# Performance work log

Measured on AMD Instinct MI355X. Metric: run time of the kernel, lower is better.

The kernel has to match this reference:

```python
import jax, jax.numpy as jnp
import numpy as np

B, T, I, H, O = 512, 2048, 4, 100, 1


def setup_inputs() -> dict:
    key = jax.random.key(0)
    k1, k2, k3, k4 = jax.random.split(key, 4)
    s_ih = 1.0 / np.sqrt(H)
    return {
        "x": jax.random.normal(k1, (B, T, I), dtype=jnp.float32),
        "W_ih": jax.random.uniform(k2, (H, I), minval=-s_ih, maxval=s_ih, dtype=jnp.float32),
        "W_hh": jax.random.uniform(k3, (H, H), minval=-s_ih, maxval=s_ih, dtype=jnp.float32),
        "W_fc": jax.random.uniform(k4, (O, H), minval=-s_ih, maxval=s_ih, dtype=jnp.float32),
        "b_fc": jnp.zeros((O,), dtype=jnp.float32),
    }


def reference(x, W_ih, W_hh, W_fc, b_fc):
    # Precompute input projections for all timesteps: [T, B, H]
    xp = jnp.einsum("bti,hi->tbh", x, W_ih)
    h0 = jnp.zeros((x.shape[0], W_hh.shape[0]), dtype=x.dtype)

    def step(h, xp_t):
        h_new = jnp.tanh(xp_t + h @ W_hh.T)
        return h_new, h_new

    _, hs = jax.lax.scan(step, h0, xp)          # hs: [T, B, H]
    hs = jnp.swapaxes(hs, 0, 1)                 # [B, T, H]
    out = jnp.einsum("bth,oh->bto", hs, W_fc) + b_fc  # [B, T, O]
    return out
```

## Files before the change

### kernel.cpp

```cpp
#include <hip/hip_runtime.h>


#define BB 512
#define TT 2048
#define II 4
#define HH 100
#define HP 104
#define CHUNK 64
#define NCH (TT / CHUNK)

__global__ __launch_bounds__(128, 1) void crnn_kernel(
    const float* __restrict__ x,
    const float* __restrict__ W_ih,
    const float* __restrict__ W_hh,
    const float* __restrict__ W_fc,
    const float* __restrict__ b_fc,
    float* __restrict__ out)
{
    __shared__ float xs[TT * II];
    __shared__ float hh[(CHUNK + 1) * HP];
    __shared__ float wfcs[HP];
    __shared__ float pt[2][CHUNK];

    const int tid = threadIdx.x;
    const int b   = blockIdx.x;
    const int j   = tid;
    const int jj  = (j < HH) ? j : HH - 1;
    const bool active = (j < HH);

    const float4* xg = reinterpret_cast<const float4*>(x + (size_t)b * TT * II);
    float4* xl = reinterpret_cast<float4*>(xs);
#pragma unroll
    for (int it = 0; it < (TT * II / 4) / 128; ++it)
        xl[it * 128 + tid] = xg[it * 128 + tid];

    float4 wih = reinterpret_cast<const float4*>(W_ih)[jj];
    float wr[HH];
    const float4* wrow = reinterpret_cast<const float4*>(W_hh + jj * HH);
#pragma unroll
    for (int k4 = 0; k4 < HH / 4; ++k4) {
        float4 v = wrow[k4];
        wr[4 * k4 + 0] = v.x; wr[4 * k4 + 1] = v.y;
        wr[4 * k4 + 2] = v.z; wr[4 * k4 + 3] = v.w;
    }
    if (tid < HP) wfcs[tid] = (tid < HH) ? W_fc[tid] : 0.f;
    const float bias = b_fc[0];
    if (tid < HP) hh[tid] = 0.f;
    for (int i = tid; i < (CHUNK + 1) * 4; i += 128) {
        int r = i >> 2, p = i & 3;
        hh[r * HP + HH + p] = 0.f;
    }
    __syncthreads();

    float* outb = out + (size_t)b * TT;
    const float4* xs4 = reinterpret_cast<const float4*>(xs);

    for (int c = 0; c < NCH; ++c) {
        for (int t = 0; t < CHUNK; ++t) {
            const float4* hrow = reinterpret_cast<const float4*>(hh + t * HP);
            float4 hv[HH / 4];
#pragma unroll
            for (int k4 = 0; k4 < HH / 4; ++k4) hv[k4] = hrow[k4];
            float4 xv = xs4[c * CHUNK + t];

            float a0 = wih.x * xv.x;
            float a1 = wih.y * xv.y;
            float a2 = wih.z * xv.z;
            float a3 = wih.w * xv.w;
#pragma unroll
            for (int k4 = 0; k4 < HH / 4; ++k4) {
                a0 = fmaf(wr[4 * k4 + 0], hv[k4].x, a0);
                a1 = fmaf(wr[4 * k4 + 1], hv[k4].y, a1);
                a2 = fmaf(wr[4 * k4 + 2], hv[k4].z, a2);
                a3 = fmaf(wr[4 * k4 + 3], hv[k4].w, a3);
            }
            float acc = (a0 + a1) + (a2 + a3);
            float e  = __expf(2.f * acc);
            float hn = 1.f - 2.f * __builtin_amdgcn_rcpf(e + 1.f);
            if (active) hh[(t + 1) * HP + j] = hn;
            __syncthreads();
        }

        const int tl = tid & (CHUNK - 1);
        const int kh = tid >> 6;
        const int k0 = kh * 52;
        const float4* wf4 = reinterpret_cast<const float4*>(wfcs + k0);
        const float4* hr  = reinterpret_cast<const float4*>(hh + (tl + 1) * HP + k0);
        float csum = 0.f;
#pragma unroll
        for (int i = 0; i < 13; ++i) {
            float4 hvv = hr[i];
            float4 wv  = wf4[i];
            csum = fmaf(hvv.x, wv.x, csum);
            csum = fmaf(hvv.y, wv.y, csum);
            csum = fmaf(hvv.z, wv.z, csum);
            csum = fmaf(hvv.w, wv.w, csum);
        }
        pt[kh][tl] = csum;
        if (tid < HH) hh[tid] = hh[CHUNK * HP + tid];
        __syncthreads();
        if (tid < CHUNK) outb[c * CHUNK + tid] = (pt[0][tid] + pt[1][tid]) + bias;
        __syncthreads();
    }
}

extern "C" void kernel_launch(void* const* d_in, const int* in_sizes, int n_in,
                              void* d_out, int out_size, void* d_ws, size_t ws_size,
                              hipStream_t stream) {
    const float* x    = (const float*)d_in[0];
    const float* W_ih = (const float*)d_in[1];
    const float* W_hh = (const float*)d_in[2];
    const float* W_fc = (const float*)d_in[3];
    const float* b_fc = (const float*)d_in[4];
    float* out = (float*)d_out;
    crnn_kernel<<<BB, 128, 0, stream>>>(x, W_ih, W_hh, W_fc, b_fc, out);
}
```

Baseline: 1.104 ms.

## Broadcast hidden state via wave readlane instead of LDS row reads

Each thread keeps its own new hidden value in a register, and the other wave's values come from a single LDS load per step. Both are broadcast to all lanes with readlane, which replaces the 25 float4 LDS reads of the whole hidden row per timestep. The hh buffer drops its extra carry row, and the copy of the last row plus one barrier per chunk are removed. The cost is about 100 scalar readlane operations on the serial dependency chain, and the padding is widened to 116.

```diff
diff --git a/kernel.cpp b/kernel.cpp
--- a/kernel.cpp
+++ b/kernel.cpp
@@ -5,9 +5,13 @@
 #define TT 2048
 #define II 4
 #define HH 100
-#define HP 104
+#define HP 116
 #define CHUNK 64
 #define NCH (TT / CHUNK)
+
+__device__ __forceinline__ float rlf(float v, int l) {
+    return __int_as_float(__builtin_amdgcn_readlane(__float_as_int(v), l));
+}
 
 __global__ __launch_bounds__(128, 1) void crnn_kernel(
     const float* __restrict__ x,
@@ -18,15 +22,17 @@
     float* __restrict__ out)
 {
     __shared__ float xs[TT * II];
-    __shared__ float hh[(CHUNK + 1) * HP];
+    __shared__ float hh[CHUNK * HP];
     __shared__ float wfcs[HP];
     __shared__ float pt[2][CHUNK];
 
-    const int tid = threadIdx.x;
-    const int b   = blockIdx.x;
-    const int j   = tid;
-    const int jj  = (j < HH) ? j : HH - 1;
-    const bool active = (j < HH);
+    const int tid  = threadIdx.x;
+    const int b    = blockIdx.x;
+    const int lane = tid & 63;
+    const int w    = tid >> 6;
+    const int j    = tid;
+    const int jj   = (j < HH) ? j : HH - 1;
+    const bool act = (j < HH);
 
     const float4* xg = reinterpret_cast<const float4*>(x + (size_t)b * TT * II);
     float4* xl = reinterpret_cast<float4*>(xs);
@@ -45,47 +51,72 @@
     }
     if (tid < HP) wfcs[tid] = (tid < HH) ? W_fc[tid] : 0.f;
     const float bias = b_fc[0];
-    if (tid < HP) hh[tid] = 0.f;
-    for (int i = tid; i < (CHUNK + 1) * 4; i += 128) {
-        int r = i >> 2, p = i & 3;
+    for (int i = tid; i < CHUNK * (HP - HH); i += 128) {
+        int r = i / (HP - HH), p = i % (HP - HH);
         hh[r * HP + HH + p] = 0.f;
     }
     __syncthreads();
 
+    const int voff = w ? lane : (64 + (lane < 36 ? lane : 35));
+
+    float vh = 0.f;
+    float vo = 0.f;
     float* outb = out + (size_t)b * TT;
-    const float4* xs4 = reinterpret_cast<const float4*>(xs);
 
     for (int c = 0; c < NCH; ++c) {
+        const float4* xs4 = reinterpret_cast<const float4*>(xs) + c * CHUNK;
         for (int t = 0; t < CHUNK; ++t) {
-            const float4* hrow = reinterpret_cast<const float4*>(hh + t * HP);
-            float4 hv[HH / 4];
-#pragma unroll
-            for (int k4 = 0; k4 < HH / 4; ++k4) hv[k4] = hrow[k4];
-            float4 xv = xs4[c * CHUNK + t];
-
+            float4 xv = xs4[t];
             float a0 = wih.x * xv.x;
             float a1 = wih.y * xv.y;
             float a2 = wih.z * xv.z;
             float a3 = wih.w * xv.w;
+            if (w == 0) {
 #pragma unroll
-            for (int k4 = 0; k4 < HH / 4; ++k4) {
-                a0 = fmaf(wr[4 * k4 + 0], hv[k4].x, a0);
-                a1 = fmaf(wr[4 * k4 + 1], hv[k4].y, a1);
-                a2 = fmaf(wr[4 * k4 + 2], hv[k4].z, a2);
-                a3 = fmaf(wr[4 * k4 + 3], hv[k4].w, a3);
+                for (int k = 0; k < 64; k += 4) {
+                    a0 = fmaf(wr[k + 0], rlf(vh, k + 0), a0);
+                    a1 = fmaf(wr[k + 1], rlf(vh, k + 1), a1);
+                    a2 = fmaf(wr[k + 2], rlf(vh, k + 2), a2);
+                    a3 = fmaf(wr[k + 3], rlf(vh, k + 3), a3);
+                }
+#pragma unroll
+                for (int k = 64; k < 100; k += 4) {
+                    a0 = fmaf(wr[k + 0], rlf(vo, k - 64 + 0), a0);
+                    a1 = fmaf(wr[k + 1], rlf(vo, k - 64 + 1), a1);
+                    a2 = fmaf(wr[k + 2], rlf(vo, k - 64 + 2), a2);
+                    a3 = fmaf(wr[k + 3], rlf(vo, k - 64 + 3), a3);
+                }
+            } else {
+#pragma unroll
+                for (int k = 64; k < 100; k += 4) {
+                    a0 = fmaf(wr[k + 0], rlf(vh, k - 64 + 0), a0);
+                    a1 = fmaf(wr[k + 1], rlf(vh, k - 64 + 1), a1);
+                    a2 = fmaf(wr[k + 2], rlf(vh, k - 64 + 2), a2);
+                    a3 = fmaf(wr[k + 3], rlf(vh, k - 64 + 3), a3);
+                }
+#pragma unroll
+                for (int k = 0; k < 64; k += 4) {
+                    a0 = fmaf(wr[k + 0], rlf(vo, k + 0), a0);
+                    a1 = fmaf(wr[k + 1], rlf(vo, k + 1), a1);
+                    a2 = fmaf(wr[k + 2], rlf(vo, k + 2), a2);
+                    a3 = fmaf(wr[k + 3], rlf(vo, k + 3), a3);
+                }
             }
             float acc = (a0 + a1) + (a2 + a3);
-            float e  = __expf(2.f * acc);
-            float hn = 1.f - 2.f * __builtin_amdgcn_rcpf(e + 1.f);
-            if (active) hh[(t + 1) * HP + j] = hn;
+            float e   = __expf(2.f * acc);
+            float hn  = 1.f - 2.f * __builtin_amdgcn_rcpf(e + 1.f);
+            vh = hn;
+            float* rowW = hh + t * HP;
+            if (act) rowW[j] = hn;
             __syncthreads();
+            vo = rowW[voff];
         }
 
         const int tl = tid & (CHUNK - 1);
         const int kh = tid >> 6;
         const int k0 = kh * 52;
         const float4* wf4 = reinterpret_cast<const float4*>(wfcs + k0);
-        const float4* hr  = reinterpret_cast<const float4*>(hh + (tl + 1) * HP + k0);
+        const float4* hr  = reinterpret_cast<const float4*>(hh + tl * HP + k0);
         float csum = 0.f;
 #pragma unroll
         for (int i = 0; i < 13; ++i) {
@@ -97,10 +128,8 @@
             csum = fmaf(hvv.w, wv.w, csum);
         }
         pt[kh][tl] = csum;
-        if (tid < HH) hh[tid] = hh[CHUNK * HP + tid];
         __syncthreads();
         if (tid < CHUNK) outb[c * CHUNK + tid] = (pt[0][tid] + pt[1][tid]) + bias;
-        __syncthreads();
     }
 }
 
```

Measured after the change: 962.6 us. 1.15x faster.
